# Performance work log

Hardware: AMD Instinct MI355X
Metric: run time of the kernel (lower is better)

The kernel has to match this reference:

```python
import jax, jax.numpy as jnp
import numpy as np

B, S, NH, HD = 2, 4096, 16, 64


def setup_inputs() -> dict:
    key = jax.random.key(0)
    kq, kk, kv = jax.random.split(key, 3)
    q = jax.random.normal(kq, (B, S, NH, HD), dtype=jnp.float32)
    k = jax.random.normal(kk, (B, S, NH, HD), dtype=jnp.float32)
    v = jax.random.normal(kv, (B, S, NH, HD), dtype=jnp.float32)
    return {"q": q, "k": k, "v": v}


def reference(q, k, v):
    # SDPA.__call__ with attention_mask=None, segment_ids=None, is_causal=True, dropout=identity
    q_len, nheads, kv_len = q.shape[-3], q.shape[-2], k.shape[-3]
    qs = q / jnp.sqrt(jnp.asarray(q.shape[-1], q.dtype))
    scores = jnp.einsum('...tnh,...snh->...tns', qs, k)  # [B, q, nheads, kv]
    # causal mask: tril over (q, kv), broadcast over heads axis (-2)
    causal = jnp.tril(jnp.ones((q_len, kv_len), dtype=jnp.bool_))[:, None, :]
    neg_inf = jnp.finfo(scores.dtype).min
    scores = jnp.where(causal, scores, neg_inf)
    weights = jax.nn.softmax(scores.astype(jnp.float32), axis=-1).astype(scores.dtype)
    attn = jnp.einsum('...tns,...snh->...tnh', weights, v)
    return attn
```

## Files before the change

kernel.cpp:

```cpp
#include <hip/hip_runtime.h>


constexpr int BATCH  = 2;
constexpr int SEQ    = 4096;
constexpr int NHEADS = 16;
constexpr int HDIM   = 64;
constexpr int BM     = 128;
constexpr int BN     = 64;
constexpr int QTILES = SEQ / BM;
constexpr int BH     = BATCH * NHEADS;

typedef __attribute__((ext_vector_type(8)))  short v8s;
typedef __attribute__((ext_vector_type(16))) float v16f;
typedef __attribute__((ext_vector_type(4)))  unsigned int v4u;

__device__ __forceinline__ unsigned pkbf(float a, float b) {
#if __has_builtin(__builtin_amdgcn_cvt_pk_bf16_f32)
    return __builtin_bit_cast(unsigned, __builtin_amdgcn_cvt_pk_bf16_f32(a, b));
#else
    unsigned ua = __float_as_uint(a); ua += 0x7FFFu + ((ua >> 16) & 1u);
    unsigned ub = __float_as_uint(b); ub += 0x7FFFu + ((ub >> 16) & 1u);
    return (ua >> 16) | (ub & 0xFFFF0000u);
#endif
}
__device__ __forceinline__ unsigned short f2bf(float x) {
    unsigned u = __float_as_uint(x);
    u += 0x7FFFu + ((u >> 16) & 1u);
    return (unsigned short)(u >> 16);
}

__device__ __forceinline__ void async16(const unsigned short* g, unsigned short* l) {
    __builtin_amdgcn_global_load_lds(
        (const __attribute__((address_space(1))) unsigned int*)g,
        (__attribute__((address_space(3))) unsigned int*)l, 16, 0, 0);
}

__global__ __launch_bounds__(256, 4)
void prepack(const float* __restrict__ q, const float* __restrict__ k,
             const float* __restrict__ v, unsigned short* __restrict__ qb,
             unsigned short* __restrict__ kb, unsigned short* __restrict__ vt)
{
    __shared__ unsigned int tl32[64 * 32];
    const int tid = threadIdx.x;
    const int s0  = blockIdx.x * 64;
    const int bh  = blockIdx.y;
    const int b = bh >> 4, h = bh & 15;
    const int row = tid >> 2, c16 = (tid & 3) * 16;
    const size_t in_off  = ((size_t)((b * SEQ + s0 + row) * NHEADS + h)) * HDIM + c16;
    const size_t out_off = ((size_t)bh * SEQ + s0 + row) * HDIM + c16;
    const float sc = 0.125f * 1.44269504088896340736f;
    {
        const float4* s4 = (const float4*)(q + in_off);
        unsigned short tmp[16];
        #pragma unroll
        for (int i = 0; i < 4; ++i) { float4 f = s4[i];
            tmp[i*4+0]=f2bf(f.x*sc); tmp[i*4+1]=f2bf(f.y*sc);
            tmp[i*4+2]=f2bf(f.z*sc); tmp[i*4+3]=f2bf(f.w*sc); }
        v8s* o = (v8s*)(qb + out_off);
        o[0] = *(const v8s*)&tmp[0]; o[1] = *(const v8s*)&tmp[8];
    }
    {
        const float4* s4 = (const float4*)(k + in_off);
        unsigned short tmp[16];
        #pragma unroll
        for (int i = 0; i < 4; ++i) { float4 f = s4[i];
            tmp[i*4+0]=f2bf(f.x); tmp[i*4+1]=f2bf(f.y);
            tmp[i*4+2]=f2bf(f.z); tmp[i*4+3]=f2bf(f.w); }
        v8s* o = (v8s*)(kb + out_off);
        o[0] = *(const v8s*)&tmp[0]; o[1] = *(const v8s*)&tmp[8];
    }
    {
        const float4* s4 = (const float4*)(v + in_off);
        #pragma unroll
        for (int i = 0; i < 4; ++i) {
            float4 f = s4[i];
            const int c2 = (c16 >> 1) + i * 2;
            tl32[row * 32 + ((c2 + 0 + row) & 31)] = pkbf(f.x, f.y);
            tl32[row * 32 + ((c2 + 1 + row) & 31)] = pkbf(f.z, f.w);
        }
    }
    __syncthreads();
    {
        const int hd = tid >> 2;
        const int hd2 = hd >> 1;
        unsigned out[8];
        #pragma unroll
        for (int i = 0; i < 8; ++i) {
            const int sca = (tid & 3) * 8 + i;
            const unsigned a  = tl32[(2*sca  ) * 32 + ((hd2 + 2*sca    ) & 31)];
            const unsigned bb = tl32[(2*sca+1) * 32 + ((hd2 + 2*sca + 1) & 31)];
            out[i] = (hd & 1) ? ((a >> 16) | (bb & 0xFFFF0000u))
                              : ((a & 0xFFFFu) | (bb << 16));
        }
        unsigned int* dst = (unsigned int*)(vt + ((size_t)bh * HDIM + hd) * SEQ + s0) + (tid & 3) * 8;
        ((v4u*)dst)[0] = (v4u){out[0], out[1], out[2], out[3]};
        ((v4u*)dst)[1] = (v4u){out[4], out[5], out[6], out[7]};
    }
}

__global__ __launch_bounds__(256, 4)
void fa_fwd(const unsigned short* __restrict__ qb, const unsigned short* __restrict__ kb,
            const unsigned short* __restrict__ vt, float* __restrict__ og)
{
    __shared__ __align__(16) unsigned short k_s[2][64 * 64];
    __shared__ __align__(16) unsigned short v_s[2][64 * 64];
    __shared__ float l_buf[BM];

    const int tid  = threadIdx.x;
    const int wave = tid >> 6;
    const int lane = tid & 63;
    const int hh   = lane >> 5;
    const int l32  = lane & 31;

    const int n  = (int)blockIdx.x;
    const int qtile = QTILES - 1 - (n >> 5);
    const int bh = n & 31;
    const int qbase = qtile * BM;
    const int jmax  = 2 * qtile + 2;

    const int lrow  = lane >> 3;
    const int lcol8 = (lane & 7) ^ lrow;

    const unsigned short* qg  = qb + ((size_t)bh * SEQ + qbase) * HDIM;
    const unsigned short* kgb = kb + (size_t)bh * SEQ * HDIM;
    const unsigned short* vgb = vt + (size_t)bh * HDIM * SEQ;

    #pragma unroll
    for (int i = 0; i < 4; ++i) {
        const int rbase = i * 32 + wave * 8;
        unsigned short* dst = (rbase < 64) ? &k_s[0][rbase * 64] : &v_s[0][(rbase - 64) * 64];
        async16(qg + (size_t)(rbase + lrow) * HDIM + lcol8 * 8, dst);
    }
    __syncthreads();

    v8s bq[4];
    {
        const int R = wave * 32 + l32;
        const unsigned short* qrow = (R < 64) ? &k_s[0][R * 64] : &v_s[0][(R - 64) * 64];
        #pragma unroll
        for (int c = 0; c < 4; ++c)
            bq[c] = *(const v8s*)&qrow[(((2*c + hh) ^ (R & 7)) * 8)];
    }
    __syncthreads();

    #pragma unroll
    for (int i = 0; i < 2; ++i) {
        const int rbase = i * 32 + wave * 8;
        async16(kgb + (size_t)(rbase + lrow) * HDIM + lcol8 * 8, &k_s[0][rbase * 64]);
        async16(vgb + (size_t)(rbase + lrow) * SEQ  + lcol8 * 8, &v_s[0][rbase * 64]);
    }

    v16f o_acc[2];
    o_acc[0] = (v16f)(0.f); o_acc[1] = (v16f)(0.f);
    float l_lane = 0.f;
    const int q_abs = qbase + wave * 32 + l32;

    for (int jt = 0; jt < jmax; ++jt) {
        const int buf = jt & 1;
        __syncthreads();

        if (jt + 1 < jmax) {
            const int nb  = (jt + 1) & 1;
            const int kb2 = (jt + 1) * BN;
            #pragma unroll
            for (int i = 0; i < 2; ++i) {
                const int rbase = i * 32 + wave * 8;
                async16(kgb + (size_t)(kb2 + rbase + lrow) * HDIM + lcol8 * 8, &k_s[nb][rbase * 64]);
                async16(vgb + (size_t)(rbase + lrow) * SEQ + kb2  + lcol8 * 8, &v_s[nb][rbase * 64]);
            }
        }

        v16f sacc[2];
        sacc[0] = (v16f)(0.f); sacc[1] = (v16f)(0.f);
        #pragma unroll
        for (int mt = 0; mt < 2; ++mt) {
            const int r = mt * 32 + l32;
            #pragma unroll
            for (int c = 0; c < 4; ++c) {
                v8s ak = *(const v8s*)&k_s[buf][r * 64 + (((2*c + hh) ^ (l32 & 7)) * 8)];
                sacc[mt] = __builtin_amdgcn_mfma_f32_32x32x16_bf16(ak, bq[c], sacc[mt], 0, 0, 0);
            }
        }

        const bool masked = (jt >= jmax - 2);
        v8s pf[4];
        #pragma unroll
        for (int mt = 0; mt < 2; ++mt) {
            #pragma unroll
            for (int r = 0; r < 16; ++r) {
                float pv = __builtin_amdgcn_exp2f(sacc[mt][r]);
                if (masked) {
                    const int k_abs = jt * 64 + mt * 32 + (r & 3) + 8 * (r >> 2) + 4 * hh;
                    pv = (k_abs > q_abs) ? 0.f : pv;
                }
                sacc[mt][r] = pv;
                l_lane += pv;
            }
            #pragma unroll
            for (int cc = 0; cc < 2; ++cc) {
                const unsigned lo0 = pkbf(sacc[mt][8*cc+0], sacc[mt][8*cc+1]);
                const unsigned lo1 = pkbf(sacc[mt][8*cc+2], sacc[mt][8*cc+3]);
                const unsigned hi0 = pkbf(sacc[mt][8*cc+4], sacc[mt][8*cc+5]);
                const unsigned hi1 = pkbf(sacc[mt][8*cc+6], sacc[mt][8*cc+7]);
                const unsigned s0 = hh ? lo0 : hi0;
                const unsigned s1 = hh ? lo1 : hi1;
                const unsigned t0 = (unsigned)__shfl_xor((int)s0, 32, 64);
                const unsigned t1 = (unsigned)__shfl_xor((int)s1, 32, 64);
                v4u w;
                w.x = hh ? t0 : lo0;
                w.y = hh ? t1 : lo1;
                w.z = hh ? hi0 : t0;
                w.w = hh ? hi1 : t1;
                pf[mt*2 + cc] = __builtin_bit_cast(v8s, w);
            }
        }

        #pragma unroll
        for (int nt = 0; nt < 2; ++nt) {
            const int r = nt * 32 + l32;
            #pragma unroll
            for (int c = 0; c < 4; ++c) {
                v8s bv = *(const v8s*)&v_s[buf][r * 64 + (((2*c + hh) ^ (l32 & 7)) * 8)];
                o_acc[nt] = __builtin_amdgcn_mfma_f32_32x32x16_bf16(pf[c], bv, o_acc[nt], 0, 0, 0);
            }
        }
    }

    const float lt = l_lane + __shfl_xor(l_lane, 32);
    if (hh == 0) l_buf[wave * 32 + l32] = lt;
    __syncthreads();

    const int b = bh >> 4, h = bh & 15;
    #pragma unroll
    for (int r = 0; r < 16; ++r) {
        const int q_local = (r & 3) + 8 * (r >> 2) + 4 * hh;
        const float inv_l = 1.0f / l_buf[wave * 32 + q_local];
        const int qrow = qbase + wave * 32 + q_local;
        float* dst = og + ((size_t)((b * SEQ + qrow) * NHEADS + h)) * HDIM + l32;
        dst[0]  = o_acc[0][r] * inv_l;
        dst[32] = o_acc[1][r] * inv_l;
    }
}

extern "C" void kernel_launch(void* const* d_in, const int* in_sizes, int n_in,
                              void* d_out, int out_size, void* d_ws, size_t ws_size,
                              hipStream_t stream) {
    const float* q = (const float*)d_in[0];
    const float* k = (const float*)d_in[1];
    const float* v = (const float*)d_in[2];
    float* out = (float*)d_out;

    const size_t TEN = (size_t)BATCH * NHEADS * SEQ * HDIM;
    unsigned short* qbuf = (unsigned short*)d_ws;
    unsigned short* kbuf = qbuf + TEN;
    unsigned short* vbuf = kbuf + TEN;

    dim3 pgrid(SEQ / 64, BH);
    prepack<<<pgrid, 256, 0, stream>>>(q, k, v, qbuf, kbuf, vbuf);
    fa_fwd<<<QTILES * BH, 256, 0, stream>>>(qbuf, kbuf, vbuf, out);
}
```

Measured before the change: 264.2 us.

## Fuse bf16 prepack into attention kernel with register-staged K/V prefetch

Removes the separate prepack kernel and the bf16 workspace round trip. The attention kernel now reads fp32 Q/K/V directly, converts them to bf16 in registers, and writes them into swizzled LDS, transposing V in the process. The async global-to-LDS copies are replaced by register prefetch of the next tile, with the stores to LDS placed after the MFMA work. In exchange, each tile is re-read from fp32 global memory (twice the bytes) by every causal q-tile, register pressure rises, and occupancy is lowered to 3.

```diff
diff --git a/kernel.cpp b/kernel.cpp
--- a/kernel.cpp
+++ b/kernel.cpp
@@ -23,84 +23,10 @@
     return (ua >> 16) | (ub & 0xFFFF0000u);
 #endif
 }
-__device__ __forceinline__ unsigned short f2bf(float x) {
-    unsigned u = __float_as_uint(x);
-    u += 0x7FFFu + ((u >> 16) & 1u);
-    return (unsigned short)(u >> 16);
-}
-
-__device__ __forceinline__ void async16(const unsigned short* g, unsigned short* l) {
-    __builtin_amdgcn_global_load_lds(
-        (const __attribute__((address_space(1))) unsigned int*)g,
-        (__attribute__((address_space(3))) unsigned int*)l, 16, 0, 0);
-}
-
-__global__ __launch_bounds__(256, 4)
-void prepack(const float* __restrict__ q, const float* __restrict__ k,
-             const float* __restrict__ v, unsigned short* __restrict__ qb,
-             unsigned short* __restrict__ kb, unsigned short* __restrict__ vt)
-{
-    __shared__ unsigned int tl32[64 * 32];
-    const int tid = threadIdx.x;
-    const int s0  = blockIdx.x * 64;
-    const int bh  = blockIdx.y;
-    const int b = bh >> 4, h = bh & 15;
-    const int row = tid >> 2, c16 = (tid & 3) * 16;
-    const size_t in_off  = ((size_t)((b * SEQ + s0 + row) * NHEADS + h)) * HDIM + c16;
-    const size_t out_off = ((size_t)bh * SEQ + s0 + row) * HDIM + c16;
-    const float sc = 0.125f * 1.44269504088896340736f;
-    {
-        const float4* s4 = (const float4*)(q + in_off);
-        unsigned short tmp[16];
-        #pragma unroll
-        for (int i = 0; i < 4; ++i) { float4 f = s4[i];
-            tmp[i*4+0]=f2bf(f.x*sc); tmp[i*4+1]=f2bf(f.y*sc);
-            tmp[i*4+2]=f2bf(f.z*sc); tmp[i*4+3]=f2bf(f.w*sc); }
-        v8s* o = (v8s*)(qb + out_off);
-        o[0] = *(const v8s*)&tmp[0]; o[1] = *(const v8s*)&tmp[8];
-    }
-    {
-        const float4* s4 = (const float4*)(k + in_off);
-        unsigned short tmp[16];
-        #pragma unroll
-        for (int i = 0; i < 4; ++i) { float4 f = s4[i];
-            tmp[i*4+0]=f2bf(f.x); tmp[i*4+1]=f2bf(f.y);
-            tmp[i*4+2]=f2bf(f.z); tmp[i*4+3]=f2bf(f.w); }
-        v8s* o = (v8s*)(kb + out_off);
-        o[0] = *(const v8s*)&tmp[0]; o[1] = *(const v8s*)&tmp[8];
-    }
-    {
-        const float4* s4 = (const float4*)(v + in_off);
-        #pragma unroll
-        for (int i = 0; i < 4; ++i) {
-            float4 f = s4[i];
-            const int c2 = (c16 >> 1) + i * 2;
-            tl32[row * 32 + ((c2 + 0 + row) & 31)] = pkbf(f.x, f.y);
-            tl32[row * 32 + ((c2 + 1 + row) & 31)] = pkbf(f.z, f.w);
-        }
-    }
-    __syncthreads();
-    {
-        const int hd = tid >> 2;
-        const int hd2 = hd >> 1;
-        unsigned out[8];
-        #pragma unroll
-        for (int i = 0; i < 8; ++i) {
-            const int sca = (tid & 3) * 8 + i;
-            const unsigned a  = tl32[(2*sca  ) * 32 + ((hd2 + 2*sca    ) & 31)];
-            const unsigned bb = tl32[(2*sca+1) * 32 + ((hd2 + 2*sca + 1) & 31)];
-            out[i] = (hd & 1) ? ((a >> 16) | (bb & 0xFFFF0000u))
-                              : ((a & 0xFFFFu) | (bb << 16));
-        }
-        unsigned int* dst = (unsigned int*)(vt + ((size_t)bh * HDIM + hd) * SEQ + s0) + (tid & 3) * 8;
-        ((v4u*)dst)[0] = (v4u){out[0], out[1], out[2], out[3]};
-        ((v4u*)dst)[1] = (v4u){out[4], out[5], out[6], out[7]};
-    }
-}
-
-__global__ __launch_bounds__(256, 4)
-void fa_fwd(const unsigned short* __restrict__ qb, const unsigned short* __restrict__ kb,
-            const unsigned short* __restrict__ vt, float* __restrict__ og)
+
+__global__ __launch_bounds__(256, 3)
+void fa_fused(const float* __restrict__ qf, const float* __restrict__ kf,
+              const float* __restrict__ vf, float* __restrict__ og)
 {
     __shared__ __align__(16) unsigned short k_s[2][64 * 64];
     __shared__ __align__(16) unsigned short v_s[2][64 * 64];
@@ -115,24 +41,34 @@
     const int n  = (int)blockIdx.x;
     const int qtile = QTILES - 1 - (n >> 5);
     const int bh = n & 31;
+    const int b = bh >> 4, h = bh & 15;
     const int qbase = qtile * BM;
     const int jmax  = 2 * qtile + 2;
 
-    const int lrow  = lane >> 3;
-    const int lcol8 = (lane & 7) ^ lrow;
-
-    const unsigned short* qg  = qb + ((size_t)bh * SEQ + qbase) * HDIM;
-    const unsigned short* kgb = kb + (size_t)bh * SEQ * HDIM;
-    const unsigned short* vgb = vt + (size_t)bh * HDIM * SEQ;
-
-    #pragma unroll
-    for (int i = 0; i < 4; ++i) {
-        const int rbase = i * 32 + wave * 8;
-        unsigned short* dst = (rbase < 64) ? &k_s[0][rbase * 64] : &v_s[0][(rbase - 64) * 64];
-        async16(qg + (size_t)(rbase + lrow) * HDIM + lcol8 * 8, dst);
+    const int krow = tid >> 2;
+    const int kc   = (tid & 3) * 16;
+    const int sg0  = (2*(tid & 3))     ^ (krow & 7);
+    const int sg1  = (2*(tid & 3) + 1) ^ (krow & 7);
+    const int vp   = tid & 31;
+    const int vo   = tid >> 5;
+
+    const size_t rowstride = (size_t)NHEADS * HDIM;
+
+    {
+        const float sc = 0.125f * 1.44269504088896340736f;
+        #pragma unroll
+        for (int half = 0; half < 2; ++half) {
+            const float4* src = (const float4*)(qf +
+                ((size_t)((b * SEQ + qbase + half * 64 + krow) * NHEADS + h)) * HDIM + kc);
+            float4 f0 = src[0], f1 = src[1], f2 = src[2], f3 = src[3];
+            unsigned short* dst = half ? &v_s[0][krow * 64] : &k_s[0][krow * 64];
+            *(v4u*)&dst[sg0 * 8] = (v4u){pkbf(f0.x*sc, f0.y*sc), pkbf(f0.z*sc, f0.w*sc),
+                                         pkbf(f1.x*sc, f1.y*sc), pkbf(f1.z*sc, f1.w*sc)};
+            *(v4u*)&dst[sg1 * 8] = (v4u){pkbf(f2.x*sc, f2.y*sc), pkbf(f2.z*sc, f2.w*sc),
+                                         pkbf(f3.x*sc, f3.y*sc), pkbf(f3.z*sc, f3.w*sc)};
+        }
     }
     __syncthreads();
-
     v8s bq[4];
     {
         const int R = wave * 32 + l32;
@@ -143,11 +79,23 @@
     }
     __syncthreads();
 
-    #pragma unroll
-    for (int i = 0; i < 2; ++i) {
-        const int rbase = i * 32 + wave * 8;
-        async16(kgb + (size_t)(rbase + lrow) * HDIM + lcol8 * 8, &k_s[0][rbase * 64]);
-        async16(vgb + (size_t)(rbase + lrow) * SEQ  + lcol8 * 8, &v_s[0][rbase * 64]);
+    const float4* kpf = (const float4*)(kf + ((size_t)((b * SEQ + krow) * NHEADS + h)) * HDIM + kc);
+    const float4* vpf = (const float4*)(vf + ((size_t)((b * SEQ + 2*vp) * NHEADS + h)) * HDIM + 8*vo);
+    const size_t kstep = (BN * rowstride) / 4;
+    const size_t vrow1 = rowstride / 4;
+
+    {
+        float4 a0 = kpf[0], a1 = kpf[1], a2 = kpf[2], a3 = kpf[3];
+        float4 c0 = vpf[0], c1 = vpf[1], d0 = vpf[vrow1], d1 = vpf[vrow1 + 1];
+        unsigned short* kd = &k_s[0][krow * 64];
+        *(v4u*)&kd[sg0 * 8] = (v4u){pkbf(a0.x,a0.y), pkbf(a0.z,a0.w), pkbf(a1.x,a1.y), pkbf(a1.z,a1.w)};
+        *(v4u*)&kd[sg1 * 8] = (v4u){pkbf(a2.x,a2.y), pkbf(a2.z,a2.w), pkbf(a3.x,a3.y), pkbf(a3.z,a3.w)};
+        const float va[8] = {c0.x,c0.y,c0.z,c0.w, c1.x,c1.y,c1.z,c1.w};
+        const float vb[8] = {d0.x,d0.y,d0.z,d0.w, d1.x,d1.y,d1.z,d1.w};
+        unsigned int* vw = (unsigned int*)&v_s[0][0];
+        #pragma unroll
+        for (int i = 0; i < 8; ++i)
+            vw[(8*vo + i) * 32 + (((vp >> 2) ^ i) << 2) + (vp & 3)] = pkbf(va[i], vb[i]);
     }
 
     v16f o_acc[2];
@@ -159,15 +107,13 @@
         const int buf = jt & 1;
         __syncthreads();
 
-        if (jt + 1 < jmax) {
-            const int nb  = (jt + 1) & 1;
-            const int kb2 = (jt + 1) * BN;
-            #pragma unroll
-            for (int i = 0; i < 2; ++i) {
-                const int rbase = i * 32 + wave * 8;
-                async16(kgb + (size_t)(kb2 + rbase + lrow) * HDIM + lcol8 * 8, &k_s[nb][rbase * 64]);
-                async16(vgb + (size_t)(rbase + lrow) * SEQ + kb2  + lcol8 * 8, &v_s[nb][rbase * 64]);
-            }
+        const bool pf_on = (jt + 1 < jmax);
+        float4 a0, a1, a2, a3, c0, c1, d0, d1;
+        if (pf_on) {
+            const float4* kp = kpf + (size_t)(jt + 1) * kstep;
+            a0 = kp[0]; a1 = kp[1]; a2 = kp[2]; a3 = kp[3];
+            const float4* vq = vpf + (size_t)(jt + 1) * kstep;
+            c0 = vq[0]; c1 = vq[1]; d0 = vq[vrow1]; d1 = vq[vrow1 + 1];
         }
 
         v16f sacc[2];
@@ -224,13 +170,25 @@
                 o_acc[nt] = __builtin_amdgcn_mfma_f32_32x32x16_bf16(pf[c], bv, o_acc[nt], 0, 0, 0);
             }
         }
+
+        if (pf_on) {
+            const int nb = (jt + 1) & 1;
+            unsigned short* kd = &k_s[nb][krow * 64];
+            *(v4u*)&kd[sg0 * 8] = (v4u){pkbf(a0.x,a0.y), pkbf(a0.z,a0.w), pkbf(a1.x,a1.y), pkbf(a1.z,a1.w)};
+            *(v4u*)&kd[sg1 * 8] = (v4u){pkbf(a2.x,a2.y), pkbf(a2.z,a2.w), pkbf(a3.x,a3.y), pkbf(a3.z,a3.w)};
+            const float va[8] = {c0.x,c0.y,c0.z,c0.w, c1.x,c1.y,c1.z,c1.w};
+            const float vb[8] = {d0.x,d0.y,d0.z,d0.w, d1.x,d1.y,d1.z,d1.w};
+            unsigned int* vw = (unsigned int*)&v_s[nb][0];
+            #pragma unroll
+            for (int i = 0; i < 8; ++i)
+                vw[(8*vo + i) * 32 + (((vp >> 2) ^ i) << 2) + (vp & 3)] = pkbf(va[i], vb[i]);
+        }
     }
 
     const float lt = l_lane + __shfl_xor(l_lane, 32);
     if (hh == 0) l_buf[wave * 32 + l32] = lt;
     __syncthreads();
 
-    const int b = bh >> 4, h = bh & 15;
     #pragma unroll
     for (int r = 0; r < 16; ++r) {
         const int q_local = (r & 3) + 8 * (r >> 2) + 4 * hh;
@@ -249,13 +207,5 @@
     const float* k = (const float*)d_in[1];
     const float* v = (const float*)d_in[2];
     float* out = (float*)d_out;
-
-    const size_t TEN = (size_t)BATCH * NHEADS * SEQ * HDIM;
-    unsigned short* qbuf = (unsigned short*)d_ws;
-    unsigned short* kbuf = qbuf + TEN;
-    unsigned short* vbuf = kbuf + TEN;
-
-    dim3 pgrid(SEQ / 64, BH);
-    prepack<<<pgrid, 256, 0, stream>>>(q, k, v, qbuf, kbuf, vbuf);
-    fa_fwd<<<QTILES * BH, 256, 0, stream>>>(qbuf, kbuf, vbuf, out);
+    fa_fused<<<QTILES * BH, 256, 0, stream>>>(q, k, v, out);
 }
```

Measured after the change: 359.4 us. +36.0%, slower.
